# Performance work log

Measured on AMD Instinct MI355X. Metric: run time of the kernel, lower is better.

The kernel has to match this reference:

```python
import jax, jax.numpy as jnp
import numpy as np

N_NODES = 100000
N_EDGES = 1600000
D = 128
OUT = 8


def setup_inputs() -> dict:
    key = jax.random.key(0)
    k1, k2, k3, k4 = jax.random.split(key, 4)
    h = jax.random.normal(k1, (N_NODES, D), dtype=jnp.float32)
    src = jax.random.randint(k2, (N_EDGES,), 0, N_NODES, dtype=jnp.int64)
    dst = jax.random.randint(k3, (N_EDGES,), 0, N_NODES, dtype=jnp.int64)
    W = jax.random.normal(k4, (OUT, 2 * D), dtype=jnp.float32) * (1.0 / np.sqrt(2 * D))
    b = jnp.zeros((OUT,), dtype=jnp.float32)
    return {"h": h, "src": src, "dst": dst, "W": W, "b": b}


def reference(h, src, dst, W, b):
    # Edge score = Linear(concat(h[src], h[dst])).
    # Split W to avoid materializing the concatenated [E, 2D] tensor:
    # concat(u, v) @ W.T == u @ Wu.T + v @ Wv.T
    Wu = W[:, :D]   # [OUT, D]
    Wv = W[:, D:]   # [OUT, D]
    score = (jnp.einsum('ed,od->eo', h[src], Wu)
             + jnp.einsum('ed,od->eo', h[dst], Wv)
             + b)  # [E, OUT]
    return score
```

## Files before the change

### kernel.cpp

```cpp
#include <hip/hip_runtime.h>

#define NDIM 128
#define NOUT 8

typedef float     f32x4 __attribute__((ext_vector_type(4)));
typedef _Float16  f16x8 __attribute__((ext_vector_type(8)));

__global__ __launch_bounds__(256) void node_proj_kernel(
    const float* __restrict__ h, const float* __restrict__ W,
    const float* __restrict__ b, _Float16* __restrict__ P, int n_nodes) {
  const int lane = threadIdx.x & 63;
  const int wv   = threadIdx.x >> 6;
  const int nb   = blockIdx.x * 64 + wv * 16;
  const int c    = lane & 15;
  const int kg   = lane >> 4;

  const float* __restrict__ wp =
      W + (c & 7) * (2 * NDIM) + (c >> 3) * NDIM + kg * 8;
  f16x8 bf[4];
#pragma unroll
  for (int s = 0; s < 4; ++s) {
    const f32x4 w0 = *reinterpret_cast<const f32x4*>(wp + s * 32);
    const f32x4 w1 = *reinterpret_cast<const f32x4*>(wp + s * 32 + 4);
    f16x8 t;
    t[0] = (_Float16)w0.x; t[1] = (_Float16)w0.y;
    t[2] = (_Float16)w0.z; t[3] = (_Float16)w0.w;
    t[4] = (_Float16)w1.x; t[5] = (_Float16)w1.y;
    t[6] = (_Float16)w1.z; t[7] = (_Float16)w1.w;
    bf[s] = t;
  }

  const int node = nb + c;
  const bool valid = node < n_nodes;
  const float* __restrict__ hp = h + (size_t)node * NDIM + kg * 8;

  f32x4 acc = {0.f, 0.f, 0.f, 0.f};
#pragma unroll
  for (int s = 0; s < 4; ++s) {
    f16x8 af = {};
    if (valid) {
      const f32x4 a0 = *reinterpret_cast<const f32x4*>(hp + s * 32);
      const f32x4 a1 = *reinterpret_cast<const f32x4*>(hp + s * 32 + 4);
      af[0] = (_Float16)a0.x; af[1] = (_Float16)a0.y;
      af[2] = (_Float16)a0.z; af[3] = (_Float16)a0.w;
      af[4] = (_Float16)a1.x; af[5] = (_Float16)a1.y;
      af[6] = (_Float16)a1.z; af[7] = (_Float16)a1.w;
    }
    acc = __builtin_amdgcn_mfma_f32_16x16x32_f16(af, bf[s], acc, 0, 0, 0);
  }

  const float bias = (c >= 8) ? b[c - 8] : 0.f;
#pragma unroll
  for (int i = 0; i < 4; ++i) {
    const int nrow = nb + kg * 4 + i;
    if (nrow < n_nodes)
      P[(size_t)nrow * 16 + c] = (_Float16)(acc[i] + bias);
  }
}

__global__ __launch_bounds__(256) void edge_score_kernel(
    const int* __restrict__ src, const int* __restrict__ dst,
    const _Float16* __restrict__ P, float* __restrict__ out, int n_edges) {
  const int t = threadIdx.x;
  const int e0 = blockIdx.x * 512 + t;
  const int e1 = e0 + 256;
  const bool v0 = e0 < n_edges;
  const bool v1 = e1 < n_edges;

  const f16x8* __restrict__ Pp = reinterpret_cast<const f16x8*>(P);
  f32x4* __restrict__ op = reinterpret_cast<f32x4*>(out);

  int s0 = 0, d0 = 0, s1 = 0, d1 = 0;
  if (v0) {
    s0 = __builtin_nontemporal_load(src + e0);
    d0 = __builtin_nontemporal_load(dst + e0);
  }
  if (v1) {
    s1 = __builtin_nontemporal_load(src + e1);
    d1 = __builtin_nontemporal_load(dst + e1);
  }

  if (v0) {
    const f16x8 sv = Pp[(size_t)s0 * 2 + 0];
    const f16x8 dv = Pp[(size_t)d0 * 2 + 1];
    f32x4 r0, r1;
    r0.x = (float)sv[0] + (float)dv[0]; r0.y = (float)sv[1] + (float)dv[1];
    r0.z = (float)sv[2] + (float)dv[2]; r0.w = (float)sv[3] + (float)dv[3];
    r1.x = (float)sv[4] + (float)dv[4]; r1.y = (float)sv[5] + (float)dv[5];
    r1.z = (float)sv[6] + (float)dv[6]; r1.w = (float)sv[7] + (float)dv[7];
    __builtin_nontemporal_store(r0, op + (size_t)e0 * 2 + 0);
    __builtin_nontemporal_store(r1, op + (size_t)e0 * 2 + 1);
  }
  if (v1) {
    const f16x8 sv = Pp[(size_t)s1 * 2 + 0];
    const f16x8 dv = Pp[(size_t)d1 * 2 + 1];
    f32x4 r0, r1;
    r0.x = (float)sv[0] + (float)dv[0]; r0.y = (float)sv[1] + (float)dv[1];
    r0.z = (float)sv[2] + (float)dv[2]; r0.w = (float)sv[3] + (float)dv[3];
    r1.x = (float)sv[4] + (float)dv[4]; r1.y = (float)sv[5] + (float)dv[5];
    r1.z = (float)sv[6] + (float)dv[6]; r1.w = (float)sv[7] + (float)dv[7];
    __builtin_nontemporal_store(r0, op + (size_t)e1 * 2 + 0);
    __builtin_nontemporal_store(r1, op + (size_t)e1 * 2 + 1);
  }
}

__global__ __launch_bounds__(256) void edge_direct_kernel(
    const float* __restrict__ h, const int* __restrict__ src,
    const int* __restrict__ dst, const float* __restrict__ W,
    const float* __restrict__ b, float* __restrict__ out, int n_edges) {
  const int e = blockIdx.x * 256 + threadIdx.x;
  if (e >= n_edges) return;
  const int s = src[e];
  const int d = dst[e];
  const float4* __restrict__ hs = reinterpret_cast<const float4*>(h + (size_t)s * NDIM);
  const float4* __restrict__ hd = reinterpret_cast<const float4*>(h + (size_t)d * NDIM);
  const float4* __restrict__ W4 = reinterpret_cast<const float4*>(W);

  float acc[NOUT];
#pragma unroll
  for (int o = 0; o < NOUT; ++o) acc[o] = b[o];

  for (int j = 0; j < 32; ++j) {
    const float4 vs = hs[j];
    const float4 vd = hd[j];
#pragma unroll
    for (int o = 0; o < NOUT; ++o) {
      const float4 wu = W4[o * 64 + j];
      const float4 wv = W4[o * 64 + 32 + j];
      acc[o] = fmaf(vs.x, wu.x, fmaf(vs.y, wu.y, fmaf(vs.z, wu.z, fmaf(vs.w, wu.w, acc[o]))));
      acc[o] = fmaf(vd.x, wv.x, fmaf(vd.y, wv.y, fmaf(vd.z, wv.z, fmaf(vd.w, wv.w, acc[o]))));
    }
  }

  float4 r0, r1;
  r0.x = acc[0]; r0.y = acc[1]; r0.z = acc[2]; r0.w = acc[3];
  r1.x = acc[4]; r1.y = acc[5]; r1.z = acc[6]; r1.w = acc[7];
  float4* __restrict__ op = reinterpret_cast<float4*>(out + (size_t)e * NOUT);
  op[0] = r0;
  op[1] = r1;
}

extern "C" void kernel_launch(void* const* d_in, const int* in_sizes, int n_in,
                              void* d_out, int out_size, void* d_ws, size_t ws_size,
                              hipStream_t stream) {
  const float* h   = (const float*)d_in[0];
  const int*   src = (const int*)d_in[1];
  const int*   dst = (const int*)d_in[2];
  const float* W   = (const float*)d_in[3];
  const float* b   = (const float*)d_in[4];
  float* out = (float*)d_out;

  const int n_nodes = in_sizes[0] / NDIM;
  const int n_edges = in_sizes[1];

  const size_t need = (size_t)n_nodes * 16 * sizeof(_Float16);
  if (ws_size >= need) {
    _Float16* P = (_Float16*)d_ws;
    node_proj_kernel<<<(n_nodes + 63) / 64, 256, 0, stream>>>(h, W, b, P, n_nodes);
    edge_score_kernel<<<(n_edges + 511) / 512, 256, 0, stream>>>(src, dst, P, out, n_edges);
  } else {
    edge_direct_kernel<<<(n_edges + 255) / 256, 256, 0, stream>>>(h, src, dst, W, b, out, n_edges);
  }
}
```

Measured before the change: 47.38 us.

## Make node projection persistent with double-buffered tile prefetch

The node projection kernel now runs on a fixed grid of 512 blocks. Each wave loops over 16-node tiles with a grid stride and prefetches the next tile's h rows into a second register buffer while the current tile's MFMA and stores run. The aim is to keep memory requests in flight continuously and avoid launching thousands of short-lived blocks. In exchange it uses more registers, and with a fixed grid size the kernel may underfill or unevenly load the GPU.

Result: faster. 43.07 us (-9.1%).

```diff
diff --git a/kernel.cpp b/kernel.cpp
--- a/kernel.cpp
+++ b/kernel.cpp
@@ -11,7 +11,6 @@
     const float* __restrict__ b, _Float16* __restrict__ P, int n_nodes) {
   const int lane = threadIdx.x & 63;
   const int wv   = threadIdx.x >> 6;
-  const int nb   = blockIdx.x * 64 + wv * 16;
   const int c    = lane & 15;
   const int kg   = lane >> 4;
 
@@ -30,31 +29,57 @@
     bf[s] = t;
   }
 
-  const int node = nb + c;
-  const bool valid = node < n_nodes;
-  const float* __restrict__ hp = h + (size_t)node * NDIM + kg * 8;
+  const int ntile   = (n_nodes + 15) >> 4;
+  const int wstride = gridDim.x * 4;
+  const int nmax    = n_nodes - 1;
+  const float bias  = (c >= 8) ? b[c - 8] : 0.f;
 
-  f32x4 acc = {0.f, 0.f, 0.f, 0.f};
+  auto load_tile = [&](int tile, f32x4 (&a)[8]) {
+    const int node = min(tile * 16 + c, nmax);
+    const float* __restrict__ hp = h + (size_t)node * NDIM + kg * 8;
 #pragma unroll
-  for (int s = 0; s < 4; ++s) {
-    f16x8 af = {};
-    if (valid) {
-      const f32x4 a0 = *reinterpret_cast<const f32x4*>(hp + s * 32);
-      const f32x4 a1 = *reinterpret_cast<const f32x4*>(hp + s * 32 + 4);
-      af[0] = (_Float16)a0.x; af[1] = (_Float16)a0.y;
-      af[2] = (_Float16)a0.z; af[3] = (_Float16)a0.w;
-      af[4] = (_Float16)a1.x; af[5] = (_Float16)a1.y;
-      af[6] = (_Float16)a1.z; af[7] = (_Float16)a1.w;
+    for (int s = 0; s < 4; ++s) {
+      a[s * 2 + 0] = *reinterpret_cast<const f32x4*>(hp + s * 32);
+      a[s * 2 + 1] = *reinterpret_cast<const f32x4*>(hp + s * 32 + 4);
     }
-    acc = __builtin_amdgcn_mfma_f32_16x16x32_f16(af, bf[s], acc, 0, 0, 0);
-  }
+  };
+  auto compute_store = [&](int tile, const f32x4 (&a)[8]) {
+    f32x4 acc = {0.f, 0.f, 0.f, 0.f};
+#pragma unroll
+    for (int s = 0; s < 4; ++s) {
+      f16x8 af;
+#pragma unroll
+      for (int j = 0; j < 4; ++j) {
+        af[j]     = (_Float16)a[s * 2 + 0][j];
+        af[j + 4] = (_Float16)a[s * 2 + 1][j];
+      }
+      acc = __builtin_amdgcn_mfma_f32_16x16x32_f16(af, bf[s], acc, 0, 0, 0);
+    }
+    const int rbase = tile * 16 + kg * 4;
+#pragma unroll
+    for (int i = 0; i < 4; ++i) {
+      const int nrow = rbase + i;
+      if (nrow < n_nodes)
+        P[(size_t)nrow * 16 + c] = (_Float16)(acc[i] + bias);
+    }
+  };
 
-  const float bias = (c >= 8) ? b[c - 8] : 0.f;
-#pragma unroll
-  for (int i = 0; i < 4; ++i) {
-    const int nrow = nb + kg * 4 + i;
-    if (nrow < n_nodes)
-      P[(size_t)nrow * 16 + c] = (_Float16)(acc[i] + bias);
+  int tile = blockIdx.x * 4 + wv;
+  if (tile >= ntile) return;
+
+  f32x4 bufA[8], bufB[8];
+  load_tile(tile, bufA);
+  while (true) {
+    const int t1 = tile + wstride;
+    if (t1 >= ntile) { compute_store(tile, bufA); break; }
+    load_tile(t1, bufB);
+    compute_store(tile, bufA);
+    tile = t1;
+    const int t2 = tile + wstride;
+    if (t2 >= ntile) { compute_store(tile, bufB); break; }
+    load_tile(t2, bufA);
+    compute_store(tile, bufB);
+    tile = t2;
   }
 }
 
@@ -156,7 +181,7 @@
   const size_t need = (size_t)n_nodes * 16 * sizeof(_Float16);
   if (ws_size >= need) {
     _Float16* P = (_Float16*)d_ws;
-    node_proj_kernel<<<(n_nodes + 63) / 64, 256, 0, stream>>>(h, W, b, P, n_nodes);
+    node_proj_kernel<<<512, 256, 0, stream>>>(h, W, b, P, n_nodes);
     edge_score_kernel<<<(n_edges + 511) / 512, 256, 0, stream>>>(src, dst, P, out, n_edges);
   } else {
     edge_direct_kernel<<<(n_edges + 255) / 256, 256, 0, stream>>>(h, src, dst, W, b, out, n_edges);
```
